# Performance work log

Hardware: AMD Instinct MI355X
Metric: run time of the kernel (lower is better)

Reference implementation:

```python
import jax, jax.numpy as jnp
import numpy as np

B, N, C, H = 2, 2048, 1024, 16
HD = C // H  # head dim = 64


def setup_inputs() -> dict:
    key = jax.random.key(0)
    kq, kk, kv, km = jax.random.split(key, 4)
    q = jax.random.normal(kq, (B, N, C), dtype=jnp.float32)
    k = jax.random.normal(kk, (B, N, C), dtype=jnp.float32)
    v = jax.random.normal(kv, (B, N, C), dtype=jnp.float32)
    mask = jax.random.randint(km, (B, 1, N, N), 0, 2, dtype=jnp.int32)
    return {"q": q, "k": k, "v": v, "mask": mask}


def reference(q, k, v, mask):
    b, n, c = q.shape
    # (B, N, C) -> (B, H, N, HD)
    qh = q.reshape(b, n, H, HD).transpose(0, 2, 1, 3)
    kh = k.reshape(b, n, H, HD).transpose(0, 2, 1, 3)
    vh = v.reshape(b, n, H, HD).transpose(0, 2, 1, 3)
    scale = 1.0 / jnp.sqrt(jnp.float32(HD))
    # scores: (B, H, N, N)
    scores = jnp.einsum("bhqd,bhkd->bhqk", qh, kh) * scale
    scores = jnp.where(mask == 0, jnp.float32(-1e9), scores)
    probs = jax.nn.softmax(scores, axis=-1)
    atten = jnp.einsum("bhqk,bhkd->bhqd", probs, vh)
    # (B, H, N, HD) -> (B, N, C)
    return atten.transpose(0, 2, 1, 3).reshape(b, n, c)
```

## Files before the change

### kernel.cpp

```cpp
#include <hip/hip_runtime.h>
#include <hip/hip_bf16.h>

#define B_ 2
#define N_ 2048
#define C_ 1024
#define H_ 16
#define HD_ 64

#define KT 64
#define NT (N_ / KT)
#define TILE_E 4096
#define PSTR 72
#define NW 8
#define QB 128

#define NWM 8
#define QBM 128

typedef short s16x8 __attribute__((ext_vector_type(8)));
typedef short s16x4 __attribute__((ext_vector_type(4)));
typedef float f32x4 __attribute__((ext_vector_type(4)));

__device__ __forceinline__ s16x8 cvt8(float4 a, float4 b) {
    union { s16x8 v; __hip_bfloat162 h[4]; } u;
    u.h[0] = __float22bfloat162_rn(float2{a.x, a.y});
    u.h[1] = __float22bfloat162_rn(float2{a.z, a.w});
    u.h[2] = __float22bfloat162_rn(float2{b.x, b.y});
    u.h[3] = __float22bfloat162_rn(float2{b.z, b.w});
    return u.v;
}

__device__ __forceinline__ void gll16(const void* g, void* l) {
    __builtin_amdgcn_global_load_lds(
        (const __attribute__((address_space(1))) unsigned*)g,
        (__attribute__((address_space(3))) unsigned*)l, 16, 0, 0);
}

__global__ __launch_bounds__(256)
void pack_mask(const int* __restrict__ M, unsigned long long* __restrict__ bits) {
    const int gw   = (blockIdx.x * 256 + threadIdx.x) >> 6;
    const int lane = threadIdx.x & 63;
#pragma unroll
    for (int it = 0; it < 16; ++it) {
        const size_t wi = (size_t)gw * 16 + it;
        unsigned long long bal = __ballot(M[wi * 64 + lane] != 0);
        if (lane == 0) bits[wi] = bal;
    }
}

__global__ __launch_bounds__(256)
void prepass(const int* __restrict__ M, const float* __restrict__ K,
             const float* __restrict__ V, unsigned long long* __restrict__ bits,
             ushort* __restrict__ Kw, ushort* __restrict__ Vw) {
    const int bid = blockIdx.x;
    const int tid = threadIdx.x;
    if (bid < 2048) {
        const int gt = bid * 256 + tid;
        const int4* src = (const int4*)M + (size_t)gt * 4;
        unsigned r = 0;
#pragma unroll
        for (int c = 0; c < 4; ++c) {
            const int4 m4 = src[c];
            r |= (m4.x != 0 ? 1u : 0u) << (c * 4 + 0);
            r |= (m4.y != 0 ? 1u : 0u) << (c * 4 + 1);
            r |= (m4.z != 0 ? 1u : 0u) << (c * 4 + 2);
            r |= (m4.w != 0 ? 1u : 0u) << (c * 4 + 3);
        }
        ((ushort*)bits)[gt] = (ushort)r;
    } else if (bid < 4096) {
        const int gt = (bid - 2048) * 256 + tid;
        const int b  = gt >> 18;
        const int h  = (gt >> 14) & 15;
        const int n  = (gt >> 3) & 2047;
        const int db = gt & 7;
        const size_t src = (size_t)(b * N_ + n) * C_ + h * 64 + db * 8;
        float4 f0 = *(const float4*)(K + src);
        float4 f1 = *(const float4*)(K + src + 4);
        const int key = n & 63, kt = n >> 6;
        const int p = (key & 32) | ((key & 4) << 2) | ((key >> 1) & 12) | (key & 3);
        ushort* dst = Kw + (size_t)((b * H_ + h) * NT + kt) * TILE_E
                         + p * 64 + ((db ^ (p & 7)) * 8);
        *(s16x8*)dst = cvt8(f0, f1);
    } else {
        const int gt  = (bid - 4096) * 256 + tid;
        const int b   = gt >> 16;
        const int h   = (gt >> 12) & 15;
        const int kt  = (gt >> 7) & 31;
        const int kb4 = (gt >> 3) & 15;
        const int db  = gt & 7;
        const int key0 = kb4 * 4;
        float f[4][8];
#pragma unroll
        for (int i = 0; i < 4; ++i) {
            const size_t src = (size_t)(b * N_ + kt * 64 + key0 + i) * C_ + h * 64 + db * 8;
            *(float4*)&f[i][0] = *(const float4*)(V + src);
            *(float4*)&f[i][4] = *(const float4*)(V + src + 4);
        }
        ushort* tb = Vw + (size_t)((b * H_ + h) * NT + kt) * TILE_E;
#pragma unroll
        for (int j = 0; j < 8; ++j) {
            const int d = db * 8 + j;
            union { s16x4 v; __hip_bfloat162 h2[2]; } u;
            u.h2[0] = __float22bfloat162_rn(float2{f[0][j], f[1][j]});
            u.h2[1] = __float22bfloat162_rn(float2{f[2][j], f[3][j]});
            *(s16x4*)(tb + d * 64 + (((key0 >> 3) ^ (d & 7)) * 8) + (key0 & 7)) = u.v;
        }
    }
}

__global__ __launch_bounds__(512, 2)
void mha_fwd(const float* __restrict__ Q, const ushort* __restrict__ Kw,
             const ushort* __restrict__ Vw, const unsigned* __restrict__ bits,
             float* __restrict__ O) {
    __shared__ ushort Kl[2][TILE_E];
    __shared__ ushort Vt[2][TILE_E];

    const int sid = blockIdx.x;
    const int jj  = sid >> 3;
    const int hb  = ((sid & 7) << 2) | (jj & 3);
    const int qt  = jj >> 2;
    const int h   = hb & 15;
    const int b   = hb >> 4;

    const int tid  = threadIdx.x;
    const int w    = tid >> 6;
    const int lane = tid & 63;
    const int l16  = lane & 15;
    const int quad = lane >> 4;

    const size_t head_off = (size_t)b * N_ * C_ + (size_t)h * HD_;
    const int qb = qt * QBM + w * 16;

    const float qs = 0.125f * 1.44269504088896f;
    const size_t qoff = head_off + (size_t)(qb + l16) * C_ + quad * 8;
    float4 q0 = *(const float4*)(Q + qoff);
    float4 q1 = *(const float4*)(Q + qoff + 4);
    float4 q2 = *(const float4*)(Q + qoff + 32);
    float4 q3 = *(const float4*)(Q + qoff + 36);
    q0.x*=qs; q0.y*=qs; q0.z*=qs; q0.w*=qs;
    q1.x*=qs; q1.y*=qs; q1.z*=qs; q1.w*=qs;
    q2.x*=qs; q2.y*=qs; q2.z*=qs; q2.w*=qs;
    q3.x*=qs; q3.y*=qs; q3.z*=qs; q3.w*=qs;
    const s16x8 qa0 = cvt8(q0, q1);
    const s16x8 qa1 = cvt8(q2, q3);

    s16x8 onesb;
#pragma unroll
    for (int i = 0; i < 8; ++i) onesb[i] = (short)0x3F80;

    const f32x4 kZero = {0.f, 0.f, 0.f, 0.f};

    f32x4 acc[4];
#pragma unroll
    for (int c = 0; c < 4; ++c) acc[c] = f32x4{0.f, 0.f, 0.f, 0.f};
    f32x4 sum = f32x4{0.f, 0.f, 0.f, 0.f};

    const int fbase = l16 * 64 + ((quad ^ (l16 & 7)) * 8);

    const size_t tilebase = (size_t)((b * H_ + h) * NT) * TILE_E;
    const ushort* Kg = Kw + tilebase + (size_t)tid * 8;
    const ushort* Vg = Vw + tilebase + (size_t)tid * 8;

    const unsigned* mq = bits + ((size_t)b * N_ + qb + l16) * (N_ / 32);

    gll16(Kg, &Kl[0][w * 512]);
    gll16(Vg, &Vt[0][w * 512]);
    const ushort* Kg_pf = Kg + TILE_E;
    const ushort* Vg_pf = Vg + TILE_E;

    uint4 mw = *(const uint4*)mq;  mq += 4;

    for (int kt2 = 0; kt2 < NT; kt2 += 2) {
        const bool pf1 = (kt2 + 2 < NT);
        uint4 mw_nxt = mw;
        if (pf1) { mw_nxt = *(const uint4*)mq; }
        mq += 4;
#pragma unroll
        for (int u = 0; u < 2; ++u) {
            __syncthreads();
            if (u == 0 || pf1) {
                gll16(Kg_pf, &Kl[1 - u][w * 512]);
                gll16(Vg_pf, &Vt[1 - u][w * 512]);
                Kg_pf += TILE_E;  Vg_pf += TILE_E;
            }
            const unsigned w0 = u ? mw.z : mw.x;
            const unsigned w1 = u ? mw.w : mw.y;

            f32x4 s[4];
            __builtin_amdgcn_s_setprio(1);
#pragma unroll
            for (int t = 0; t < 4; ++t) {
                s16x8 kb0 = *(const s16x8*)(&Kl[u][fbase + t * 1024]);
                s16x8 kb1 = *(const s16x8*)(&Kl[u][(fbase ^ 32) + t * 1024]);
                f32x4 z = __builtin_amdgcn_mfma_f32_16x16x32_bf16(kb0, qa0, kZero, 0, 0, 0);
                z = __builtin_amdgcn_mfma_f32_16x16x32_bf16(kb1, qa1, z, 0, 0, 0);
                s[t] = z;
            }
            __builtin_amdgcn_s_setprio(0);

            const unsigned aw0 = w0 >> (quad * 8);
            const unsigned aw1 = w1 >> (quad * 8);
            union { s16x8 v; __hip_bfloat162 h2[4]; } pk0, pk1;
#pragma unroll
            for (int t = 0; t < 4; ++t) {
                const unsigned aw = ((t < 2) ? aw0 : aw1) >> ((t & 1) * 4);
                float p0 = __builtin_amdgcn_exp2f(((aw >> 0) & 1u) ? s[t][0] : -1e9f);
                float p1 = __builtin_amdgcn_exp2f(((aw >> 1) & 1u) ? s[t][1] : -1e9f);
                float p2 = __builtin_amdgcn_exp2f(((aw >> 2) & 1u) ? s[t][2] : -1e9f);
                float p3 = __builtin_amdgcn_exp2f(((aw >> 3) & 1u) ? s[t][3] : -1e9f);
                __hip_bfloat162 lo = __float22bfloat162_rn(float2{p0, p1});
                __hip_bfloat162 hi = __float22bfloat162_rn(float2{p2, p3});
                if      (t == 0) { pk0.h2[0] = lo; pk0.h2[1] = hi; }
                else if (t == 1) { pk0.h2[2] = lo; pk0.h2[3] = hi; }
                else if (t == 2) { pk1.h2[0] = lo; pk1.h2[1] = hi; }
                else             { pk1.h2[2] = lo; pk1.h2[3] = hi; }
            }

            __builtin_amdgcn_s_setprio(1);
#pragma unroll
            for (int half = 0; half < 2; ++half) {
                const s16x8 pa = half ? pk1.v : pk0.v;
#pragma unroll
                for (int c = 0; c < 4; ++c) {
                    const int vidx = (half ? (fbase ^ 32) : fbase) + c * 1024;
                    s16x8 vb = *(const s16x8*)(&Vt[u][vidx]);
                    acc[c] = __builtin_amdgcn_mfma_f32_16x16x32_bf16(pa, vb, acc[c], 0, 0, 0);
                }
                sum = __builtin_amdgcn_mfma_f32_16x16x32_bf16(pa, onesb, sum, 0, 0, 0);
            }
            __builtin_amdgcn_s_setprio(0);
        }
        mw = mw_nxt;
    }

#pragma unroll
    for (int r = 0; r < 4; ++r) {
        const float inv = 1.0f / sum[r];
        const size_t obase = head_off + (size_t)(qb + quad * 4 + r) * C_;
        O[obase + l16]      = acc[0][r] * inv;
        O[obase + l16 + 16] = acc[1][r] * inv;
        O[obase + l16 + 32] = acc[2][r] * inv;
        O[obase + l16 + 48] = acc[3][r] * inv;
    }
}

#define KSTR 72
#define VSTR 72
__global__ __launch_bounds__(512, 4)
void mha_fwd_fb(const float* __restrict__ Q, const float* __restrict__ K,
                const float* __restrict__ V, const unsigned* __restrict__ bits,
                float* __restrict__ O) {
    __shared__ ushort Kl[2][KT * KSTR];
    __shared__ ushort Vt[2][HD_ * VSTR];
    __shared__ ushort Pl[NW][16 * PSTR];
    const int qt = blockIdx.x, h = blockIdx.y, b = blockIdx.z, tid = threadIdx.x;
    const int w = tid >> 6, lane = tid & 63, l16 = lane & 15, quad = lane >> 4;
    const size_t head_off = (size_t)b * N_ * C_ + (size_t)h * HD_;
    const int qb = qt * QB + w * 16;
    const float qs = 0.125f * 1.44269504088896f;
    const size_t qoff = head_off + (size_t)(qb + l16) * C_ + quad * 8;
    float4 q0 = *(const float4*)(Q + qoff);
    float4 q1 = *(const float4*)(Q + qoff + 4);
    float4 q2 = *(const float4*)(Q + qoff + 32);
    float4 q3 = *(const float4*)(Q + qoff + 36);
    q0.x*=qs; q0.y*=qs; q0.z*=qs; q0.w*=qs;
    q1.x*=qs; q1.y*=qs; q1.z*=qs; q1.w*=qs;
    q2.x*=qs; q2.y*=qs; q2.z*=qs; q2.w*=qs;
    q3.x*=qs; q3.y*=qs; q3.z*=qs; q3.w*=qs;
    const s16x8 qa0 = cvt8(q0, q1);
    const s16x8 qa1 = cvt8(q2, q3);
    f32x4 acc[4];
#pragma unroll
    for (int c = 0; c < 4; ++c) acc[c] = f32x4{0.f, 0.f, 0.f, 0.f};
    float lsum = 0.f;
    const int skey = tid >> 3, sd0 = (tid & 7) * 8;
    const int kp = tid >> 4, vd0 = (tid & 15) * 4;
    const int vcol = 2 * (kp & 3) + ((((kp >> 2) ^ (vd0 >> 3)) & 7) << 3);
    const unsigned* brow = bits + ((size_t)b * N_ + qb + l16) * (N_ / 32);
    const float SHIFT = 16.0f;
    {
        const size_t kbase = head_off + (size_t)skey * C_ + sd0;
        float4 kA = *(const float4*)(K + kbase);
        float4 kB = *(const float4*)(K + kbase + 4);
        *(s16x8*)(&Kl[0][skey * KSTR + sd0]) = cvt8(kA, kB);
        const size_t vbase = head_off + (size_t)(2 * kp) * C_ + vd0;
        float4 vA = *(const float4*)(V + vbase);
        float4 vB = *(const float4*)(V + vbase + C_);
        const float* ap = (const float*)&vA;
        const float* bp = (const float*)&vB;
#pragma unroll
        for (int i = 0; i < 4; ++i) {
            __hip_bfloat162 pr = __float22bfloat162_rn(float2{ap[i], bp[i]});
            *(unsigned*)(&Vt[0][(vd0 + i) * VSTR + vcol]) = *(unsigned*)&pr;
        }
    }
    for (int kt = 0; kt < NT; ++kt) {
        const int cur = kt & 1;
        float4 kA, kB, vA, vB;
        const bool has_next = (kt + 1 < NT);
        if (has_next) {
            const size_t kbase = head_off + (size_t)((kt + 1) * KT + skey) * C_ + sd0;
            kA = *(const float4*)(K + kbase);
            kB = *(const float4*)(K + kbase + 4);
            const size_t vbase = head_off + (size_t)((kt + 1) * KT + 2 * kp) * C_ + vd0;
            vA = *(const float4*)(V + vbase);
            vB = *(const float4*)(V + vbase + C_);
        }
        const unsigned w0 = brow[2 * kt];
        const unsigned w1 = brow[2 * kt + 1];
        __syncthreads();
        f32x4 s[4];
#pragma unroll
        for (int t = 0; t < 4; ++t) {
            s16x8 kb0 = *(const s16x8*)(&Kl[cur][(t * 16 + l16) * KSTR + quad * 8]);
            s16x8 kb1 = *(const s16x8*)(&Kl[cur][(t * 16 + l16) * KSTR + quad * 8 + 32]);
            f32x4 z = {0.f, 0.f, 0.f, 0.f};
            z = __builtin_amdgcn_mfma_f32_16x16x32_bf16(kb0, qa0, z, 0, 0, 0);
            z = __builtin_amdgcn_mfma_f32_16x16x32_bf16(kb1, qa1, z, 0, 0, 0);
            s[t] = z;
        }
        const unsigned a0 = w0 >> (quad * 4);
        const unsigned a1 = w1 >> (quad * 4);
#pragma unroll
        for (int t = 0; t < 4; ++t) {
            const unsigned aw = (t < 2) ? a0 : a1;
            const int sh = (t & 1) * 16;
            float p0 = exp2f((((aw >> (sh + 0)) & 1u) ? s[t][0] : -1e9f) - SHIFT);
            float p1 = exp2f((((aw >> (sh + 1)) & 1u) ? s[t][1] : -1e9f) - SHIFT);
            float p2 = exp2f((((aw >> (sh + 2)) & 1u) ? s[t][2] : -1e9f) - SHIFT);
            float p3 = exp2f((((aw >> (sh + 3)) & 1u) ? s[t][3] : -1e9f) - SHIFT);
            lsum += (p0 + p1) + (p2 + p3);
            union { s16x4 v; __hip_bfloat162 h2[2]; } uu;
            uu.h2[0] = __float22bfloat162_rn(float2{p0, p1});
            uu.h2[1] = __float22bfloat162_rn(float2{p2, p3});
            *(s16x4*)(&Pl[w][l16 * PSTR + t * 16 + quad * 4]) = uu.v;
        }
#pragma unroll
        for (int half = 0; half < 2; ++half) {
            s16x8 pa = *(const s16x8*)(&Pl[w][l16 * PSTR + half * 32 + quad * 8]);
#pragma unroll
            for (int c = 0; c < 4; ++c) {
                const int dr = c * 16 + l16;
                const int blk = (half * 4 + quad) ^ ((dr >> 3) & 7);
                s16x8 vb = *(const s16x8*)(&Vt[cur][dr * VSTR + blk * 8]);
                acc[c] = __builtin_amdgcn_mfma_f32_16x16x32_bf16(pa, vb, acc[c], 0, 0, 0);
            }
        }
        if (has_next) {
            *(s16x8*)(&Kl[1 - cur][skey * KSTR + sd0]) = cvt8(kA, kB);
            const float* ap = (const float*)&vA;
            const float* bp = (const float*)&vB;
#pragma unroll
            for (int i = 0; i < 4; ++i) {
                __hip_bfloat162 pr = __float22bfloat162_rn(float2{ap[i], bp[i]});
                *(unsigned*)(&Vt[1 - cur][(vd0 + i) * VSTR + vcol]) = *(unsigned*)&pr;
            }
        }
    }
    lsum += __shfl_xor(lsum, 16);
    lsum += __shfl_xor(lsum, 32);
#pragma unroll
    for (int r = 0; r < 4; ++r) {
        const float inv = 1.0f / __shfl(lsum, quad * 4 + r);
        const size_t obase = head_off + (size_t)(qb + quad * 4 + r) * C_;
        O[obase + l16]      = acc[0][r] * inv;
        O[obase + l16 + 16] = acc[1][r] * inv;
        O[obase + l16 + 32] = acc[2][r] * inv;
        O[obase + l16 + 48] = acc[3][r] * inv;
    }
}

extern "C" void kernel_launch(void* const* d_in, const int* in_sizes, int n_in,
                              void* d_out, int out_size, void* d_ws, size_t ws_size,
                              hipStream_t stream) {
    const float* q = (const float*)d_in[0];
    const float* k = (const float*)d_in[1];
    const float* v = (const float*)d_in[2];
    const int*   m = (const int*)d_in[3];
    float*       o = (float*)d_out;

    const size_t BITS_BYTES = (size_t)B_ * N_ * N_ / 8;
    const size_t KV_BYTES   = (size_t)B_ * H_ * N_ * HD_ * 2;
    const size_t NEED       = BITS_BYTES + 2 * KV_BYTES;

    unsigned long long* bits = (unsigned long long*)d_ws;

    if (ws_size >= NEED) {
        ushort* kw = (ushort*)((char*)d_ws + BITS_BYTES);
        ushort* vw = (ushort*)((char*)d_ws + BITS_BYTES + KV_BYTES);
        hipLaunchKernelGGL(prepass, dim3(4608), dim3(256), 0, stream,
                           m, k, v, bits, kw, vw);
        hipLaunchKernelGGL(mha_fwd, dim3(512), dim3(512), 0, stream,
                           q, kw, vw, (const unsigned*)bits, o);
    } else {
        hipLaunchKernelGGL(pack_mask, dim3(2048), dim3(256), 0, stream, m, bits);
        dim3 grid(N_ / QB, H_, B_);
        hipLaunchKernelGGL(mha_fwd_fb, grid, dim3(512), 0, stream,
                           q, k, v, (const unsigned*)bits, o);
    }
}
```

Before: 162.4 us.

## Use 1024-thread blocks with an 8-slot LDS ring and four-tile barrier steps

The attention kernel now runs 16 waves per block covering 256 query rows, with a 256-block grid instead of 512. K and V tiles go into an 8-tile LDS ring. Each barrier step prefetches four tiles ahead and then computes four tiles, so there is one __syncthreads per four key tiles instead of one per tile. The cost is 128KB of LDS, occupancy limited to one block per CU, and more register pressure from the deeper unrolling.

```diff
diff --git a/kernel.cpp b/kernel.cpp
--- a/kernel.cpp
+++ b/kernel.cpp
@@ -14,8 +14,8 @@
 #define NW 8
 #define QB 128
 
-#define NWM 8
-#define QBM 128
+#define NWM 16
+#define QBM 256
 
 typedef short s16x8 __attribute__((ext_vector_type(8)));
 typedef short s16x4 __attribute__((ext_vector_type(4)));
@@ -108,12 +108,12 @@
     }
 }
 
-__global__ __launch_bounds__(512, 2)
+__global__ __launch_bounds__(1024, 1)
 void mha_fwd(const float* __restrict__ Q, const ushort* __restrict__ Kw,
              const ushort* __restrict__ Vw, const unsigned* __restrict__ bits,
              float* __restrict__ O) {
-    __shared__ ushort Kl[2][TILE_E];
-    __shared__ ushort Vt[2][TILE_E];
+    __shared__ ushort Kl[8][TILE_E];
+    __shared__ ushort Vt[8][TILE_E];
 
     const int sid = blockIdx.x;
     const int jj  = sid >> 3;
@@ -163,35 +163,49 @@
 
     const unsigned* mq = bits + ((size_t)b * N_ + qb + l16) * (N_ / 32);
 
-    gll16(Kg, &Kl[0][w * 512]);
-    gll16(Vg, &Vt[0][w * 512]);
-    const ushort* Kg_pf = Kg + TILE_E;
-    const ushort* Vg_pf = Vg + TILE_E;
-
-    uint4 mw = *(const uint4*)mq;  mq += 4;
-
-    for (int kt2 = 0; kt2 < NT; kt2 += 2) {
-        const bool pf1 = (kt2 + 2 < NT);
-        uint4 mw_nxt = mw;
-        if (pf1) { mw_nxt = *(const uint4*)mq; }
-        mq += 4;
-#pragma unroll
-        for (int u = 0; u < 2; ++u) {
-            __syncthreads();
-            if (u == 0 || pf1) {
-                gll16(Kg_pf, &Kl[1 - u][w * 512]);
-                gll16(Vg_pf, &Vt[1 - u][w * 512]);
-                Kg_pf += TILE_E;  Vg_pf += TILE_E;
-            }
-            const unsigned w0 = u ? mw.z : mw.x;
-            const unsigned w1 = u ? mw.w : mw.y;
+    gll16(Kg,              &Kl[0][w * 512]);
+    gll16(Kg + 2 * TILE_E, &Kl[2][w * 512]);
+    gll16(Vg,              &Vt[0][w * 512]);
+    gll16(Vg + 2 * TILE_E, &Vt[2][w * 512]);
+    const ushort* Kg_pf = Kg + 4 * TILE_E;
+    const ushort* Vg_pf = Vg + 4 * TILE_E;
+
+    uint4 mA = *(const uint4*)mq;
+    uint4 mB = *(const uint4*)(mq + 4);
+    mq += 8;
+
+    for (int kt4 = 0; kt4 < NT; kt4 += 4) {
+        const bool pf = (kt4 + 4 < NT);
+        uint4 mA_n = mA, mB_n = mB;
+        if (pf) { mA_n = *(const uint4*)mq; mB_n = *(const uint4*)(mq + 4); }
+        mq += 8;
+
+        __syncthreads();
+        if (pf) {
+            const int s0 = (kt4 + 4) & 7;
+            const int s2 = (kt4 + 6) & 7;
+            gll16(Kg_pf,              &Kl[s0][w * 512]);
+            gll16(Kg_pf + 2 * TILE_E, &Kl[s2][w * 512]);
+            gll16(Vg_pf,              &Vt[s0][w * 512]);
+            gll16(Vg_pf + 2 * TILE_E, &Vt[s2][w * 512]);
+            Kg_pf += 4 * TILE_E;  Vg_pf += 4 * TILE_E;
+        }
+
+#pragma unroll
+        for (int u = 0; u < 4; ++u) {
+            const ushort* Kb = &Kl[(kt4 + u) & 7][0];
+            const ushort* Vb = &Vt[(kt4 + u) & 7][0];
+            const unsigned w0 = (u == 0) ? mA.x : (u == 1) ? mA.z
+                               : (u == 2) ? mB.x : mB.z;
+            const unsigned w1 = (u == 0) ? mA.y : (u == 1) ? mA.w
+                               : (u == 2) ? mB.y : mB.w;
 
             f32x4 s[4];
             __builtin_amdgcn_s_setprio(1);
 #pragma unroll
             for (int t = 0; t < 4; ++t) {
-                s16x8 kb0 = *(const s16x8*)(&Kl[u][fbase + t * 1024]);
-                s16x8 kb1 = *(const s16x8*)(&Kl[u][(fbase ^ 32) + t * 1024]);
+                s16x8 kb0 = *(const s16x8*)(Kb + fbase + t * 1024);
+                s16x8 kb1 = *(const s16x8*)(Kb + (fbase ^ 32) + t * 1024);
                 f32x4 z = __builtin_amdgcn_mfma_f32_16x16x32_bf16(kb0, qa0, kZero, 0, 0, 0);
                 z = __builtin_amdgcn_mfma_f32_16x16x32_bf16(kb1, qa1, z, 0, 0, 0);
                 s[t] = z;
@@ -223,14 +237,14 @@
 #pragma unroll
                 for (int c = 0; c < 4; ++c) {
                     const int vidx = (half ? (fbase ^ 32) : fbase) + c * 1024;
-                    s16x8 vb = *(const s16x8*)(&Vt[u][vidx]);
+                    s16x8 vb = *(const s16x8*)(Vb + vidx);
                     acc[c] = __builtin_amdgcn_mfma_f32_16x16x32_bf16(pa, vb, acc[c], 0, 0, 0);
                 }
                 sum = __builtin_amdgcn_mfma_f32_16x16x32_bf16(pa, onesb, sum, 0, 0, 0);
             }
             __builtin_amdgcn_s_setprio(0);
         }
-        mw = mw_nxt;
+        mA = mA_n;  mB = mB_n;
     }
 
 #pragma unroll
@@ -390,7 +404,7 @@
         ushort* vw = (ushort*)((char*)d_ws + BITS_BYTES + KV_BYTES);
         hipLaunchKernelGGL(prepass, dim3(4608), dim3(256), 0, stream,
                            m, k, v, bits, kw, vw);
-        hipLaunchKernelGGL(mha_fwd, dim3(512), dim3(512), 0, stream,
+        hipLaunchKernelGGL(mha_fwd, dim3(256), dim3(1024), 0, stream,
                            q, kw, vw, (const unsigned*)bits, o);
     } else {
         hipLaunchKernelGGL(pack_mask, dim3(2048), dim3(256), 0, stream, m, bits);
```

After: 159.8 us. No clear change (-1.6%).
